# Performance work log

Measured on AMD Instinct MI355X. Metric: run time of the kernel, lower is better.

Reference implementation:

```python
import jax, jax.numpy as jnp
import numpy as np

D_MODEL = 1024
NUM_HEADS = 16
HEAD_DIM = D_MODEL // NUM_HEADS
T = 4096


def setup_inputs() -> dict:
    key = jax.random.key(0)
    x = jax.random.normal(key, (T, D_MODEL), dtype=jnp.float32)
    return {"x": x}


def reference(x) -> jnp.ndarray:
    T_, _ = x.shape
    # q = k = v = x reshaped to [heads, T, head_dim]
    qkv = x.reshape(T_, NUM_HEADS, HEAD_DIM).transpose(1, 0, 2)  # [H, T, hd]
    scale = 1.0 / (HEAD_DIM ** 0.5)
    scores = jnp.einsum('htd,hsd->hts', qkv, qkv) * scale  # [H, T, T]
    attn = jax.nn.softmax(scores, axis=-1)
    out = jnp.einsum('hts,hsd->htd', attn, qkv)  # [H, T, hd]
    return out.transpose(1, 0, 2).reshape(T_, D_MODEL)
```

## Files before the change

kernel.cpp:

```cpp
#include <hip/hip_runtime.h>
#include <hip/hip_bf16.h>

#define T_SEQ 4096
#define DMODEL 1024
#define NHEADS 16
#define HDIM 64
#define QBLK 128
#define SBLK 64
#define NTILES (T_SEQ / SBLK)

#define KV_BYTES ((size_t)NHEADS * NTILES * 16384)

typedef __attribute__((ext_vector_type(8))) __bf16 bf16x8;
typedef __attribute__((ext_vector_type(4))) __bf16 bf16x4;
typedef __attribute__((ext_vector_type(16))) float f32x16;
typedef __attribute__((ext_vector_type(2))) unsigned uint32x2;
typedef __attribute__((ext_vector_type(8))) unsigned short ushort8;

#define SWZ(row, col) ((col) ^ (((row) & 7) << 3))

#define QSCALE 0.1803368801111204f

__device__ __forceinline__ unsigned cvt_pk_bf16(float lo, float hi) {
  unsigned r;
  asm("v_cvt_pk_bf16_f32 %0, %1, %2" : "=v"(r) : "v"(lo), "v"(hi));
  return r;
}
__device__ __forceinline__ uint32x2 plswap(unsigned a, unsigned b) {
  return __builtin_amdgcn_permlane32_swap(a, b, false, false);
}
__device__ __forceinline__ float xhalf_max(float v) {
  uint32x2 r = plswap(__float_as_uint(v), __float_as_uint(v));
  return fmaxf(__uint_as_float(r[0]), __uint_as_float(r[1]));
}
__device__ __forceinline__ float xhalf_sum(float v) {
  uint32x2 r = plswap(__float_as_uint(v), __float_as_uint(v));
  return __uint_as_float(r[0]) + __uint_as_float(r[1]);
}
__device__ __forceinline__ void glds16(const void* g, void* l) {
  __builtin_amdgcn_global_load_lds(
      (const __attribute__((address_space(1))) unsigned int*)g,
      (__attribute__((address_space(3))) unsigned int*)l, 16, 0, 0);
}

__global__ __launch_bounds__(256) void prepass_kernel(
    const float* __restrict__ x, unsigned char* __restrict__ kvimg) {
  const int tid = threadIdx.x;
  const int c4 = tid & 15, s4 = tid >> 4;
  const int t = blockIdx.x & (NTILES - 1), h = blockIdx.x >> 6;
  const float* src = x + (size_t)(t * SBLK + s4 * 4) * DMODEL + h * HDIM + c4 * 4;
  float4 r0 = *reinterpret_cast<const float4*>(src);
  float4 r1 = *reinterpret_cast<const float4*>(src + DMODEL);
  float4 r2 = *reinterpret_cast<const float4*>(src + 2 * DMODEL);
  float4 r3 = *reinterpret_cast<const float4*>(src + 3 * DMODEL);
  __bf16 b[4][4];
  b[0][0] = (__bf16)r0.x; b[0][1] = (__bf16)r0.y; b[0][2] = (__bf16)r0.z; b[0][3] = (__bf16)r0.w;
  b[1][0] = (__bf16)r1.x; b[1][1] = (__bf16)r1.y; b[1][2] = (__bf16)r1.z; b[1][3] = (__bf16)r1.w;
  b[2][0] = (__bf16)r2.x; b[2][1] = (__bf16)r2.y; b[2][2] = (__bf16)r2.z; b[2][3] = (__bf16)r2.w;
  b[3][0] = (__bf16)r3.x; b[3][1] = (__bf16)r3.y; b[3][2] = (__bf16)r3.z; b[3][3] = (__bf16)r3.w;
  __bf16* Kimg = (__bf16*)(kvimg + (size_t)blockIdx.x * 16384);
  __bf16* Vimg = Kimg + 4096;
  #pragma unroll
  for (int j = 0; j < 4; j++) {
    const int s = s4 * 4 + j;
    bf16x4 kv; kv[0] = b[j][0]; kv[1] = b[j][1]; kv[2] = b[j][2]; kv[3] = b[j][3];
    *reinterpret_cast<bf16x4*>(&Kimg[s * 64 + SWZ(s, c4 * 4)]) = kv;
  }
  #pragma unroll
  for (int i = 0; i < 4; i++) {
    const int d = c4 * 4 + i;
    bf16x4 vv; vv[0] = b[0][i]; vv[1] = b[1][i]; vv[2] = b[2][i]; vv[3] = b[3][i];
    *reinterpret_cast<bf16x4*>(&Vimg[d * 64 + SWZ(d, s4 * 4)]) = vv;
  }
}

__global__ __launch_bounds__(256, 4) void attn_main_kernel(
    const float* __restrict__ x, const unsigned char* __restrict__ kvimg,
    float* __restrict__ outbuf) {
  const int tid  = threadIdx.x;
  const int wave = tid >> 6;
  const int lane = tid & 63;
  const int lq   = lane & 31;
  const int hi   = lane >> 5;

  const int qt = blockIdx.x & 31;
  const int h  = blockIdx.x >> 5;

  __shared__ __align__(16) unsigned char kvbytes[2][16384];

  bf16x8 qf[4];
  const int qrow = qt * QBLK + wave * 32 + lq;
  {
    const float* qp = x + (size_t)qrow * DMODEL + h * HDIM;
    #pragma unroll
    for (int ds = 0; ds < 4; ds++) {
      float4 a = *reinterpret_cast<const float4*>(qp + ds * 16 + hi * 8);
      float4 b = *reinterpret_cast<const float4*>(qp + ds * 16 + hi * 8 + 4);
      bf16x8 f;
      f[0] = (__bf16)(QSCALE * a.x); f[1] = (__bf16)(QSCALE * a.y);
      f[2] = (__bf16)(QSCALE * a.z); f[3] = (__bf16)(QSCALE * a.w);
      f[4] = (__bf16)(QSCALE * b.x); f[5] = (__bf16)(QSCALE * b.y);
      f[6] = (__bf16)(QSCALE * b.z); f[7] = (__bf16)(QSCALE * b.w);
      qf[ds] = f;
    }
  }

  const ushort8 ov = {0x3F80, 0x3F80, 0x3F80, 0x3F80,
                      0x3F80, 0x3F80, 0x3F80, 0x3F80};
  const bf16x8 ones = *reinterpret_cast<const bf16x8*>(&ov);

  f32x16 oacc[2], lacc;
  #pragma unroll
  for (int dt = 0; dt < 2; dt++)
    #pragma unroll
    for (int r = 0; r < 16; r++) oacc[dt][r] = 0.f;
  #pragma unroll
  for (int r = 0; r < 16; r++) lacc[r] = 0.f;

  const unsigned char* tbase = kvimg + ((size_t)h * NTILES * 16384);

  auto STAGE = [&](int buf, int t) {
    const unsigned char* g = tbase + (size_t)t * 16384;
    #pragma unroll
    for (int i = 0; i < 4; i++)
      glds16(g + i * 4096 + tid * 16, &kvbytes[buf][i * 4096 + tid * 16]);
  };

  STAGE(0, 0);
  __syncthreads();
  int cur = 0;

  for (int t = 0; t < NTILES; t++) {
    if (t + 1 < NTILES) STAGE(cur ^ 1, t + 1);
    const __bf16 (*Kl)[64] = reinterpret_cast<const __bf16(*)[64]>(&kvbytes[cur][0]);
    const __bf16 (*Vt)[64] = reinterpret_cast<const __bf16(*)[64]>(&kvbytes[cur][8192]);

    f32x16 sacc[2];
    #pragma unroll
    for (int kt = 0; kt < 2; kt++)
      #pragma unroll
      for (int r = 0; r < 16; r++) sacc[kt][r] = 0.f;
    __builtin_amdgcn_s_setprio(1);
    #pragma unroll
    for (int kt = 0; kt < 2; kt++) {
      #pragma unroll
      for (int ds = 0; ds < 4; ds++) {
        bf16x8 kb = *reinterpret_cast<const bf16x8*>(
            &Kl[kt * 32 + lq][SWZ(lq, ds * 16 + hi * 8)]);
        sacc[kt] = __builtin_amdgcn_mfma_f32_32x32x16_bf16(
            kb, qf[ds], sacc[kt], 0, 0, 0);
      }
    }
    __builtin_amdgcn_s_setprio(0);

    #pragma unroll
    for (int kt = 0; kt < 2; kt++)
      #pragma unroll
      for (int r = 0; r < 16; r++)
        sacc[kt][r] = __builtin_amdgcn_exp2f(sacc[kt][r]);

    bf16x8 pf[4];
    #pragma unroll
    for (int kt = 0; kt < 2; kt++) {
      #pragma unroll
      for (int b2 = 0; b2 < 2; b2++) {
        const int base = 8 * b2;
        unsigned dA0 = cvt_pk_bf16(sacc[kt][base + 0], sacc[kt][base + 1]);
        unsigned dA1 = cvt_pk_bf16(sacc[kt][base + 2], sacc[kt][base + 3]);
        unsigned dB0 = cvt_pk_bf16(sacc[kt][base + 4], sacc[kt][base + 5]);
        unsigned dB1 = cvt_pk_bf16(sacc[kt][base + 6], sacc[kt][base + 7]);
        uint32x2 r0 = plswap(dA0, dB0);
        uint32x2 r1 = plswap(dA1, dB1);
        uint4 u; u.x = r0[0]; u.y = r1[0]; u.z = r0[1]; u.w = r1[1];
        pf[kt * 2 + b2] = *reinterpret_cast<bf16x8*>(&u);
      }
    }

    __builtin_amdgcn_s_setprio(1);
    #pragma unroll
    for (int ks = 0; ks < 4; ks++)
      lacc = __builtin_amdgcn_mfma_f32_32x32x16_bf16(ones, pf[ks], lacc, 0, 0, 0);
    #pragma unroll
    for (int dt = 0; dt < 2; dt++) {
      #pragma unroll
      for (int ks = 0; ks < 4; ks++) {
        bf16x8 vb = *reinterpret_cast<const bf16x8*>(
            &Vt[dt * 32 + lq][SWZ(lq, ks * 16 + hi * 8)]);
        oacc[dt] = __builtin_amdgcn_mfma_f32_32x32x16_bf16(
            vb, pf[ks], oacc[dt], 0, 0, 0);
      }
    }
    __builtin_amdgcn_s_setprio(0);

    __syncthreads();
    cur ^= 1;
  }

  const float inv = 1.f / lacc[0];
  float* orow = outbuf + (size_t)qrow * DMODEL + h * HDIM;
  #pragma unroll
  for (int dt = 0; dt < 2; dt++) {
    #pragma unroll
    for (int m = 0; m < 4; m++) {
      float4 o;
      o.x = oacc[dt][4 * m + 0] * inv; o.y = oacc[dt][4 * m + 1] * inv;
      o.z = oacc[dt][4 * m + 2] * inv; o.w = oacc[dt][4 * m + 3] * inv;
      *reinterpret_cast<float4*>(&orow[dt * 32 + 8 * m + 4 * hi]) = o;
    }
  }
}

__global__ __launch_bounds__(256) void attn_fallback_kernel(
    const float* __restrict__ x, float* __restrict__ out) {
  const int tid  = threadIdx.x;
  const int wave = tid >> 6;
  const int lane = tid & 63;
  const int lq   = lane & 31;
  const int hi   = lane >> 5;
  const int qt = blockIdx.x & 31;
  const int h  = blockIdx.x >> 5;
  __shared__ __bf16 Kl[SBLK][HDIM];
  __shared__ __bf16 Vt[HDIM][SBLK];
  bf16x8 qf[4];
  const int qrow = qt * 128 + wave * 32 + lq;
  {
    const float* qp = x + (size_t)qrow * DMODEL + h * HDIM;
    #pragma unroll
    for (int ds = 0; ds < 4; ds++) {
      float4 a = *reinterpret_cast<const float4*>(qp + ds * 16 + hi * 8);
      float4 b = *reinterpret_cast<const float4*>(qp + ds * 16 + hi * 8 + 4);
      bf16x8 f;
      f[0] = (__bf16)(QSCALE * a.x); f[1] = (__bf16)(QSCALE * a.y);
      f[2] = (__bf16)(QSCALE * a.z); f[3] = (__bf16)(QSCALE * a.w);
      f[4] = (__bf16)(QSCALE * b.x); f[5] = (__bf16)(QSCALE * b.y);
      f[6] = (__bf16)(QSCALE * b.z); f[7] = (__bf16)(QSCALE * b.w);
      qf[ds] = f;
    }
  }
  float m_run = -1e30f, l_run = 0.f;
  f32x16 oacc[2];
  #pragma unroll
  for (int dt = 0; dt < 2; dt++)
    #pragma unroll
    for (int r = 0; r < 16; r++) oacc[dt][r] = 0.f;
  const float* xh = x + h * HDIM;
  const int c4 = tid & 15;
  const int s4 = tid >> 4;
  for (int t0 = 0; t0 < T_SEQ; t0 += SBLK) {
    __syncthreads();
    {
      const float* src = xh + (size_t)(t0 + s4 * 4) * DMODEL + c4 * 4;
      float4 r0 = *reinterpret_cast<const float4*>(src);
      float4 r1 = *reinterpret_cast<const float4*>(src + DMODEL);
      float4 r2 = *reinterpret_cast<const float4*>(src + 2 * DMODEL);
      float4 r3 = *reinterpret_cast<const float4*>(src + 3 * DMODEL);
      __bf16 b[4][4];
      b[0][0] = (__bf16)r0.x; b[0][1] = (__bf16)r0.y; b[0][2] = (__bf16)r0.z; b[0][3] = (__bf16)r0.w;
      b[1][0] = (__bf16)r1.x; b[1][1] = (__bf16)r1.y; b[1][2] = (__bf16)r1.z; b[1][3] = (__bf16)r1.w;
      b[2][0] = (__bf16)r2.x; b[2][1] = (__bf16)r2.y; b[2][2] = (__bf16)r2.z; b[2][3] = (__bf16)r2.w;
      b[3][0] = (__bf16)r3.x; b[3][1] = (__bf16)r3.y; b[3][2] = (__bf16)r3.z; b[3][3] = (__bf16)r3.w;
      #pragma unroll
      for (int j = 0; j < 4; j++) {
        const int s = s4 * 4 + j;
        bf16x4 kv; kv[0] = b[j][0]; kv[1] = b[j][1]; kv[2] = b[j][2]; kv[3] = b[j][3];
        *reinterpret_cast<bf16x4*>(&Kl[s][SWZ(s, c4 * 4)]) = kv;
      }
      #pragma unroll
      for (int i = 0; i < 4; i++) {
        const int d = c4 * 4 + i;
        bf16x4 vv; vv[0] = b[0][i]; vv[1] = b[1][i]; vv[2] = b[2][i]; vv[3] = b[3][i];
        *reinterpret_cast<bf16x4*>(&Vt[d][SWZ(d, s4 * 4)]) = vv;
      }
    }
    __syncthreads();
    f32x16 sacc[2];
    #pragma unroll
    for (int kt = 0; kt < 2; kt++)
      #pragma unroll
      for (int r = 0; r < 16; r++) sacc[kt][r] = 0.f;
    #pragma unroll
    for (int kt = 0; kt < 2; kt++) {
      #pragma unroll
      for (int ds = 0; ds < 4; ds++) {
        bf16x8 kb = *reinterpret_cast<const bf16x8*>(
            &Kl[kt * 32 + lq][SWZ(lq, ds * 16 + hi * 8)]);
        sacc[kt] = __builtin_amdgcn_mfma_f32_32x32x16_bf16(
            kb, qf[ds], sacc[kt], 0, 0, 0);
      }
    }
    float mx = sacc[0][0];
    #pragma unroll
    for (int kt = 0; kt < 2; kt++)
      #pragma unroll
      for (int r = 0; r < 16; r++) mx = fmaxf(mx, sacc[kt][r]);
    mx = xhalf_max(mx);
    const float mn = fmaxf(m_run, mx);
    const float corr = __builtin_amdgcn_exp2f(m_run - mn);
    #pragma unroll
    for (int dt = 0; dt < 2; dt++)
      #pragma unroll
      for (int r = 0; r < 16; r++) oacc[dt][r] *= corr;
    l_run *= corr;
    m_run = mn;
    float rs = 0.f;
    #pragma unroll
    for (int kt = 0; kt < 2; kt++)
      #pragma unroll
      for (int r = 0; r < 16; r++) {
        float p = __builtin_amdgcn_exp2f(sacc[kt][r] - mn);
        sacc[kt][r] = p;
        rs += p;
      }
    l_run += xhalf_sum(rs);
    bf16x8 pf[4];
    #pragma unroll
    for (int kt = 0; kt < 2; kt++) {
      #pragma unroll
      for (int b2 = 0; b2 < 2; b2++) {
        const int base = 8 * b2;
        unsigned dA0 = cvt_pk_bf16(sacc[kt][base + 0], sacc[kt][base + 1]);
        unsigned dA1 = cvt_pk_bf16(sacc[kt][base + 2], sacc[kt][base + 3]);
        unsigned dB0 = cvt_pk_bf16(sacc[kt][base + 4], sacc[kt][base + 5]);
        unsigned dB1 = cvt_pk_bf16(sacc[kt][base + 6], sacc[kt][base + 7]);
        uint32x2 r0 = plswap(dA0, dB0);
        uint32x2 r1 = plswap(dA1, dB1);
        uint4 u; u.x = r0[0]; u.y = r1[0]; u.z = r0[1]; u.w = r1[1];
        pf[kt * 2 + b2] = *reinterpret_cast<bf16x8*>(&u);
      }
    }
    #pragma unroll
    for (int dt = 0; dt < 2; dt++) {
      #pragma unroll
      for (int ks = 0; ks < 4; ks++) {
        bf16x8 vb = *reinterpret_cast<const bf16x8*>(
            &Vt[dt * 32 + lq][SWZ(lq, ks * 16 + hi * 8)]);
        oacc[dt] = __builtin_amdgcn_mfma_f32_32x32x16_bf16(
            vb, pf[ks], oacc[dt], 0, 0, 0);
      }
    }
  }
  const float inv = 1.f / l_run;
  float* orow = out + (size_t)qrow * DMODEL + h * HDIM;
  #pragma unroll
  for (int dt = 0; dt < 2; dt++) {
    #pragma unroll
    for (int m = 0; m < 4; m++) {
      float4 o;
      o.x = oacc[dt][4 * m + 0] * inv; o.y = oacc[dt][4 * m + 1] * inv;
      o.z = oacc[dt][4 * m + 2] * inv; o.w = oacc[dt][4 * m + 3] * inv;
      *reinterpret_cast<float4*>(&orow[dt * 32 + 8 * m + 4 * hi]) = o;
    }
  }
}

extern "C" void kernel_launch(void* const* d_in, const int* in_sizes, int n_in,
                              void* d_out, int out_size, void* d_ws, size_t ws_size,
                              hipStream_t stream) {
  const float* x = (const float*)d_in[0];
  float* out = (float*)d_out;
  if (ws_size >= KV_BYTES) {
    unsigned char* kvimg = (unsigned char*)d_ws;
    prepass_kernel<<<NHEADS * NTILES, 256, 0, stream>>>(x, kvimg);
    attn_main_kernel<<<NHEADS * (T_SEQ / QBLK), 256, 0, stream>>>(x, kvimg, out);
  } else {
    attn_fallback_kernel<<<NHEADS * (T_SEQ / 128), 256, 0, stream>>>(x, out);
  }
}
```

Before: 147.4 us.

## Double per-wave query rows and split key range across two blocks with merge

Each wave now handles two 32-row query subtiles, so every K/V fragment read from LDS feeds twice as many MFMAs and per-block global staging per output row is halved. The key sequence is split in two along a second grid dimension, keeping the block count unchanged. Each split writes unnormalized partial outputs and row sums to workspace, and a new merge kernel adds them and normalizes. The trade-offs are higher register pressure (occupancy bound lowered to 2), an extra kernel with about 48MB of global traffic, and a larger workspace requirement that falls back to the slow kernel if unmet.

```diff
diff --git a/kernel.cpp b/kernel.cpp
--- a/kernel.cpp
+++ b/kernel.cpp
@@ -5,11 +5,16 @@
 #define DMODEL 1024
 #define NHEADS 16
 #define HDIM 64
-#define QBLK 128
+#define QBLK 256
 #define SBLK 64
 #define NTILES (T_SEQ / SBLK)
+#define KSPLIT 2
+#define TILES_PER_SPLIT (NTILES / KSPLIT)
 
 #define KV_BYTES ((size_t)NHEADS * NTILES * 16384)
+#define P_BYTES  ((size_t)KSPLIT * T_SEQ * DMODEL * 4)
+#define L_BYTES  ((size_t)KSPLIT * NHEADS * T_SEQ * 4)
+#define WS_NEEDED (KV_BYTES + P_BYTES + L_BYTES)
 
 typedef __attribute__((ext_vector_type(8))) __bf16 bf16x8;
 typedef __attribute__((ext_vector_type(4))) __bf16 bf16x4;
@@ -74,24 +79,26 @@
   }
 }
 
-__global__ __launch_bounds__(256, 4) void attn_main_kernel(
+__global__ __launch_bounds__(256, 2) void attn_main_kernel(
     const float* __restrict__ x, const unsigned char* __restrict__ kvimg,
-    float* __restrict__ outbuf) {
+    float* __restrict__ pbuf, float* __restrict__ lbuf) {
   const int tid  = threadIdx.x;
   const int wave = tid >> 6;
   const int lane = tid & 63;
   const int lq   = lane & 31;
   const int hi   = lane >> 5;
 
-  const int qt = blockIdx.x & 31;
-  const int h  = blockIdx.x >> 5;
+  const int qt = blockIdx.x & 15;
+  const int h  = blockIdx.x >> 4;
+  const int sp = blockIdx.y;
 
   __shared__ __align__(16) unsigned char kvbytes[2][16384];
 
-  bf16x8 qf[4];
-  const int qrow = qt * QBLK + wave * 32 + lq;
-  {
-    const float* qp = x + (size_t)qrow * DMODEL + h * HDIM;
+  bf16x8 qf[2][4];
+  const int qrow0 = qt * QBLK + wave * 64 + lq;
+  #pragma unroll
+  for (int qs = 0; qs < 2; qs++) {
+    const float* qp = x + (size_t)(qrow0 + qs * 32) * DMODEL + h * HDIM;
     #pragma unroll
     for (int ds = 0; ds < 4; ds++) {
       float4 a = *reinterpret_cast<const float4*>(qp + ds * 16 + hi * 8);
@@ -101,7 +108,7 @@
       f[2] = (__bf16)(QSCALE * a.z); f[3] = (__bf16)(QSCALE * a.w);
       f[4] = (__bf16)(QSCALE * b.x); f[5] = (__bf16)(QSCALE * b.y);
       f[6] = (__bf16)(QSCALE * b.z); f[7] = (__bf16)(QSCALE * b.w);
-      qf[ds] = f;
+      qf[qs][ds] = f;
     }
   }
 
@@ -109,15 +116,19 @@
                       0x3F80, 0x3F80, 0x3F80, 0x3F80};
   const bf16x8 ones = *reinterpret_cast<const bf16x8*>(&ov);
 
-  f32x16 oacc[2], lacc;
-  #pragma unroll
-  for (int dt = 0; dt < 2; dt++)
-    #pragma unroll
-    for (int r = 0; r < 16; r++) oacc[dt][r] = 0.f;
-  #pragma unroll
-  for (int r = 0; r < 16; r++) lacc[r] = 0.f;
-
-  const unsigned char* tbase = kvimg + ((size_t)h * NTILES * 16384);
+  f32x16 oacc[2][2], lacc[2];
+  #pragma unroll
+  for (int qs = 0; qs < 2; qs++) {
+    #pragma unroll
+    for (int dt = 0; dt < 2; dt++)
+      #pragma unroll
+      for (int r = 0; r < 16; r++) oacc[qs][dt][r] = 0.f;
+    #pragma unroll
+    for (int r = 0; r < 16; r++) lacc[qs][r] = 0.f;
+  }
+
+  const unsigned char* tbase =
+      kvimg + ((size_t)(h * NTILES + sp * TILES_PER_SPLIT) * 16384);
 
   auto STAGE = [&](int buf, int t) {
     const unsigned char* g = tbase + (size_t)t * 16384;
@@ -130,16 +141,18 @@
   __syncthreads();
   int cur = 0;
 
-  for (int t = 0; t < NTILES; t++) {
-    if (t + 1 < NTILES) STAGE(cur ^ 1, t + 1);
+  for (int t = 0; t < TILES_PER_SPLIT; t++) {
+    if (t + 1 < TILES_PER_SPLIT) STAGE(cur ^ 1, t + 1);
     const __bf16 (*Kl)[64] = reinterpret_cast<const __bf16(*)[64]>(&kvbytes[cur][0]);
     const __bf16 (*Vt)[64] = reinterpret_cast<const __bf16(*)[64]>(&kvbytes[cur][8192]);
 
-    f32x16 sacc[2];
-    #pragma unroll
-    for (int kt = 0; kt < 2; kt++)
-      #pragma unroll
-      for (int r = 0; r < 16; r++) sacc[kt][r] = 0.f;
+    f32x16 sacc[2][2];
+    #pragma unroll
+    for (int qs = 0; qs < 2; qs++)
+      #pragma unroll
+      for (int kt = 0; kt < 2; kt++)
+        #pragma unroll
+        for (int r = 0; r < 16; r++) sacc[qs][kt][r] = 0.f;
     __builtin_amdgcn_s_setprio(1);
     #pragma unroll
     for (int kt = 0; kt < 2; kt++) {
@@ -147,47 +160,59 @@
       for (int ds = 0; ds < 4; ds++) {
         bf16x8 kb = *reinterpret_cast<const bf16x8*>(
             &Kl[kt * 32 + lq][SWZ(lq, ds * 16 + hi * 8)]);
-        sacc[kt] = __builtin_amdgcn_mfma_f32_32x32x16_bf16(
-            kb, qf[ds], sacc[kt], 0, 0, 0);
+        #pragma unroll
+        for (int qs = 0; qs < 2; qs++)
+          sacc[qs][kt] = __builtin_amdgcn_mfma_f32_32x32x16_bf16(
+              kb, qf[qs][ds], sacc[qs][kt], 0, 0, 0);
       }
     }
     __builtin_amdgcn_s_setprio(0);
 
     #pragma unroll
-    for (int kt = 0; kt < 2; kt++)
-      #pragma unroll
-      for (int r = 0; r < 16; r++)
-        sacc[kt][r] = __builtin_amdgcn_exp2f(sacc[kt][r]);
-
-    bf16x8 pf[4];
-    #pragma unroll
-    for (int kt = 0; kt < 2; kt++) {
-      #pragma unroll
-      for (int b2 = 0; b2 < 2; b2++) {
-        const int base = 8 * b2;
-        unsigned dA0 = cvt_pk_bf16(sacc[kt][base + 0], sacc[kt][base + 1]);
-        unsigned dA1 = cvt_pk_bf16(sacc[kt][base + 2], sacc[kt][base + 3]);
-        unsigned dB0 = cvt_pk_bf16(sacc[kt][base + 4], sacc[kt][base + 5]);
-        unsigned dB1 = cvt_pk_bf16(sacc[kt][base + 6], sacc[kt][base + 7]);
-        uint32x2 r0 = plswap(dA0, dB0);
-        uint32x2 r1 = plswap(dA1, dB1);
-        uint4 u; u.x = r0[0]; u.y = r1[0]; u.z = r0[1]; u.w = r1[1];
-        pf[kt * 2 + b2] = *reinterpret_cast<bf16x8*>(&u);
+    for (int qs = 0; qs < 2; qs++)
+      #pragma unroll
+      for (int kt = 0; kt < 2; kt++)
+        #pragma unroll
+        for (int r = 0; r < 16; r++)
+          sacc[qs][kt][r] = __builtin_amdgcn_exp2f(sacc[qs][kt][r]);
+
+    bf16x8 pf[2][4];
+    #pragma unroll
+    for (int qs = 0; qs < 2; qs++) {
+      #pragma unroll
+      for (int kt = 0; kt < 2; kt++) {
+        #pragma unroll
+        for (int b2 = 0; b2 < 2; b2++) {
+          const int base = 8 * b2;
+          unsigned dA0 = cvt_pk_bf16(sacc[qs][kt][base + 0], sacc[qs][kt][base + 1]);
+          unsigned dA1 = cvt_pk_bf16(sacc[qs][kt][base + 2], sacc[qs][kt][base + 3]);
+          unsigned dB0 = cvt_pk_bf16(sacc[qs][kt][base + 4], sacc[qs][kt][base + 5]);
+          unsigned dB1 = cvt_pk_bf16(sacc[qs][kt][base + 6], sacc[qs][kt][base + 7]);
+          uint32x2 r0 = plswap(dA0, dB0);
+          uint32x2 r1 = plswap(dA1, dB1);
+          uint4 u; u.x = r0[0]; u.y = r1[0]; u.z = r0[1]; u.w = r1[1];
+          pf[qs][kt * 2 + b2] = *reinterpret_cast<bf16x8*>(&u);
+        }
       }
     }
 
     __builtin_amdgcn_s_setprio(1);
     #pragma unroll
-    for (int ks = 0; ks < 4; ks++)
-      lacc = __builtin_amdgcn_mfma_f32_32x32x16_bf16(ones, pf[ks], lacc, 0, 0, 0);
+    for (int qs = 0; qs < 2; qs++)
+      #pragma unroll
+      for (int ks = 0; ks < 4; ks++)
+        lacc[qs] = __builtin_amdgcn_mfma_f32_32x32x16_bf16(
+            ones, pf[qs][ks], lacc[qs], 0, 0, 0);
     #pragma unroll
     for (int dt = 0; dt < 2; dt++) {
       #pragma unroll
       for (int ks = 0; ks < 4; ks++) {
         bf16x8 vb = *reinterpret_cast<const bf16x8*>(
             &Vt[dt * 32 + lq][SWZ(lq, ks * 16 + hi * 8)]);
-        oacc[dt] = __builtin_amdgcn_mfma_f32_32x32x16_bf16(
-            vb, pf[ks], oacc[dt], 0, 0, 0);
+        #pragma unroll
+        for (int qs = 0; qs < 2; qs++)
+          oacc[qs][dt] = __builtin_amdgcn_mfma_f32_32x32x16_bf16(
+              vb, pf[qs][ks], oacc[qs][dt], 0, 0, 0);
       }
     }
     __builtin_amdgcn_s_setprio(0);
@@ -196,18 +221,43 @@
     cur ^= 1;
   }
 
-  const float inv = 1.f / lacc[0];
-  float* orow = outbuf + (size_t)qrow * DMODEL + h * HDIM;
-  #pragma unroll
-  for (int dt = 0; dt < 2; dt++) {
-    #pragma unroll
-    for (int m = 0; m < 4; m++) {
-      float4 o;
-      o.x = oacc[dt][4 * m + 0] * inv; o.y = oacc[dt][4 * m + 1] * inv;
-      o.z = oacc[dt][4 * m + 2] * inv; o.w = oacc[dt][4 * m + 3] * inv;
-      *reinterpret_cast<float4*>(&orow[dt * 32 + 8 * m + 4 * hi]) = o;
-    }
-  }
+  #pragma unroll
+  for (int qs = 0; qs < 2; qs++) {
+    const int qrow = qrow0 + qs * 32;
+    float* prow = pbuf + (size_t)sp * T_SEQ * DMODEL +
+                  (size_t)qrow * DMODEL + h * HDIM;
+    #pragma unroll
+    for (int dt = 0; dt < 2; dt++) {
+      #pragma unroll
+      for (int m = 0; m < 4; m++) {
+        float4 o;
+        o.x = oacc[qs][dt][4 * m + 0]; o.y = oacc[qs][dt][4 * m + 1];
+        o.z = oacc[qs][dt][4 * m + 2]; o.w = oacc[qs][dt][4 * m + 3];
+        *reinterpret_cast<float4*>(&prow[dt * 32 + 8 * m + 4 * hi]) = o;
+      }
+    }
+    if (hi == 0)
+      lbuf[(size_t)(sp * NHEADS + h) * T_SEQ + qrow] = lacc[qs][0];
+  }
+}
+
+__global__ __launch_bounds__(256) void merge_kernel(
+    const float* __restrict__ pbuf, const float* __restrict__ lbuf,
+    float* __restrict__ out) {
+  const int gid = blockIdx.x * 256 + threadIdx.x;
+  const int row = gid >> 8;
+  const int h = (gid & 255) >> 4;
+  const float l0 = lbuf[(size_t)h * T_SEQ + row];
+  const float l1 = lbuf[(size_t)(NHEADS + h) * T_SEQ + row];
+  const float invL = 1.f / (l0 + l1);
+  const float4 p0 = reinterpret_cast<const float4*>(pbuf)[gid];
+  const float4 p1 = reinterpret_cast<const float4*>(pbuf)[(size_t)T_SEQ * DMODEL / 4 + gid];
+  float4 o;
+  o.x = (p0.x + p1.x) * invL;
+  o.y = (p0.y + p1.y) * invL;
+  o.z = (p0.z + p1.z) * invL;
+  o.w = (p0.w + p1.w) * invL;
+  reinterpret_cast<float4*>(out)[gid] = o;
 }
 
 __global__ __launch_bounds__(256) void attn_fallback_kernel(
@@ -358,10 +408,14 @@
                               hipStream_t stream) {
   const float* x = (const float*)d_in[0];
   float* out = (float*)d_out;
-  if (ws_size >= KV_BYTES) {
+  if (ws_size >= WS_NEEDED) {
     unsigned char* kvimg = (unsigned char*)d_ws;
+    float* pbuf = (float*)(kvimg + KV_BYTES);
+    float* lbuf = (float*)(kvimg + KV_BYTES + P_BYTES);
     prepass_kernel<<<NHEADS * NTILES, 256, 0, stream>>>(x, kvimg);
-    attn_main_kernel<<<NHEADS * (T_SEQ / QBLK), 256, 0, stream>>>(x, kvimg, out);
+    dim3 grid(NHEADS * (T_SEQ / QBLK), KSPLIT);
+    attn_main_kernel<<<grid, 256, 0, stream>>>(x, kvimg, pbuf, lbuf);
+    merge_kernel<<<T_SEQ * DMODEL / 4 / 256, 256, 0, stream>>>(pbuf, lbuf, out);
   } else {
     attn_fallback_kernel<<<NHEADS * (T_SEQ / 128), 256, 0, stream>>>(x, out);
   }
```

Result: slower. 155.1 us (+5.2%).
